# Kernel tuning notes

Hardware: AMD Instinct MI355X
Metric: run time of the kernel (lower is better)

The kernel has to match this reference:

```python
import jax, jax.numpy as jnp
import numpy as np

E = 128          # out_embedding_size
N = 128          # n_atoms
B = 512          # batch
CUTOFF = 5.0
LOG_STD_MIN, LOG_STD_MAX = -20.0, 2.0


def shifted_softplus(x):
    return jax.nn.softplus(x) - jnp.log(2.0).astype(x.dtype)


def cosine_cutoff(r):
    # SchNetPack CosineCutoff: 0.5*(cos(pi*r/rc)+1) for r < rc, else 0
    return 0.5 * (jnp.cos(r * (jnp.pi / CUTOFF)) + 1.0) * (r < CUTOFF).astype(r.dtype)


def setup_inputs() -> dict:
    key = jax.random.key(0)
    ks = jax.random.split(key, 8)
    kx = jax.random.normal(ks[0], (B, N, 2 * E + 1), dtype=jnp.float32)
    positions = jax.random.uniform(ks[1], (B, N, 3), dtype=jnp.float32) * 10.0
    # prefix-ones atoms mask (molecules padded at the end), 64..128 real atoms
    num_atoms = jax.random.randint(ks[2], (B,), 64, N + 1)
    atoms_mask = (jnp.arange(N)[None, :] < num_atoms[:, None]).astype(jnp.float32)
    eval_actions = jax.random.normal(ks[3], (B, N, 3), dtype=jnp.float32) * 0.1
    Wx = jax.random.normal(ks[4], (E, E), dtype=jnp.float32) / np.sqrt(E)
    bx = jnp.zeros((E,), dtype=jnp.float32)
    Wk = jax.random.normal(ks[5], (E, E), dtype=jnp.float32) / np.sqrt(E)
    bk = jnp.zeros((E,), dtype=jnp.float32)
    return {
        "kx": kx, "positions": positions, "atoms_mask": atoms_mask,
        "action_scale": jnp.float32(1.0), "eval_actions": eval_actions,
        "Wx": Wx, "bx": bx, "Wk": Wk, "bk": bk,
    }


def reference(kx, positions, atoms_mask, action_scale, eval_actions, Wx, bx, Wk, bk):
    kx = kx * atoms_mask[..., None]
    # P[b,i,j] = pos[b,j] - pos[b,i]
    P = positions[:, None, :, :] - positions[:, :, None, :]
    # safe norm: tiny eps inside sqrt so grads are finite on the zero diagonal
    r_ij = jnp.sqrt(jnp.sum(P * P, axis=-1) + 1e-16)
    P = P / (r_ij[..., None] + 1e-8)

    x = kx[..., :E]
    k = kx[..., E:2 * E]
    actions_log_std = kx[..., 2 * E:]  # [B,N,1]

    x = shifted_softplus(x) @ Wx.T + bx
    k = jax.nn.relu(k) @ Wk.T + bk

    inv_sqrt_e = 1.0 / jnp.sqrt(jnp.float32(E))
    x = jnp.einsum('bie,bje->bij', x, x) * inv_sqrt_e
    x = (r_ij - x) * 0.5
    k = jnp.einsum('bie,bje->bij', k, k) * inv_sqrt_e
    f = x * k

    # neighborhood mask: first num_atoms rows/cols are 1 (vectorized get_nbh_mask)
    counts = jnp.sum(atoms_mask, axis=-1)              # [B]
    idx = jnp.arange(N, dtype=counts.dtype)
    valid = (idx[None, :] < counts[:, None]).astype(f.dtype)   # [B,N]
    nbh_mask = valid[:, :, None] * valid[:, None, :]           # [B,N,N]

    fcut = cosine_cutoff(r_ij) * nbh_mask
    # summation_order='to' -> sum over dim 1
    actions_mean = jnp.sum(P * (f * fcut)[..., None], axis=1)  # [B,N,3]

    # limit_actions: tanh renormalization
    actions_norm = jnp.sqrt(jnp.sum(actions_mean * actions_mean, axis=-1) + 1e-16) + 1e-8
    actions_mean = actions_mean / actions_norm[..., None] * jnp.tanh(actions_norm)[..., None]

    # training path with eval_actions supplied
    actions_log_std = jnp.clip(actions_log_std, LOG_STD_MIN, LOG_STD_MAX)
    mu = actions_mean * action_scale
    sigma = jnp.exp(actions_log_std) * action_scale   # [B,N,1], broadcasts
    actions = eval_actions
    log_prob = (-0.5 * jnp.square((actions - mu) / sigma)
                - jnp.log(sigma)
                - 0.5 * jnp.log(2.0 * jnp.pi))
    log_prob = log_prob * atoms_mask[..., None]
    log_prob = jnp.sum(log_prob, axis=(1, 2))[:, None]  # [B,1]

    actions = actions * atoms_mask[..., None]
    return actions, log_prob
```

## Files before the change

kernel.cpp:

```cpp
#include <hip/hip_runtime.h>
#include <math.h>

#define EDIM 128
#define NATOM 128
#define NBATCH 512
#define THREADS 1024
#define ROWLEN 257

typedef __attribute__((ext_vector_type(8))) short bf16x8;
typedef __attribute__((ext_vector_type(4))) float f32x4;
typedef __attribute__((ext_vector_type(4))) unsigned short u16x4;

__device__ __forceinline__ unsigned short f2bf(float f) {
    unsigned u = __float_as_uint(f);
    u += 0x7FFFu + ((u >> 16) & 1u);
    return (unsigned short)(u >> 16);
}
__device__ __forceinline__ unsigned short cvt1(float x) {
    unsigned r;
    asm("v_cvt_pk_bf16_f32 %0, %1, %1" : "=v"(r) : "v"(x));
    return (unsigned short)r;
}
__device__ __forceinline__ float fast_ssp(float x) {
    return fmaxf(x, 0.f) + __logf(1.f + __expf(-fabsf(x))) - 0.69314718055994531f;
}
__device__ __forceinline__ int swzp(int row, int cbyte, int phase) {
    return row * 256 + ((cbyte ^ phase) ^ ((row & 7) << 4));
}

#define PH 0
#define QH 32768

__global__ void wcvt_kernel(const float* __restrict__ Wx,
                            const float* __restrict__ Wk,
                            unsigned short* __restrict__ ws) {
    int g = blockIdx.x * 256 + threadIdx.x;
    const float* src = (g < 16384) ? Wx : Wk;
    ws[g] = f2bf(src[g & 16383]);
}

__global__ void __launch_bounds__(THREADS, 8)
gen_actions_kernel(const float* __restrict__ kx,
                   const float* __restrict__ pos,
                   const float* __restrict__ mask,
                   const float* __restrict__ scale_ptr,
                   const float* __restrict__ evala,
                   const float* __restrict__ bx,
                   const float* __restrict__ bk,
                   const unsigned short* __restrict__ ws,
                   float* __restrict__ out)
{
    extern __shared__ char lds[];
    __shared__ float posXs[NATOM], posYs[NATOM], posZs[NATOM], lsBs[NATOM];
    __shared__ float amBs[NATOM * 3];
    __shared__ float redBs[2];
    __shared__ int   cntBs[2];

    const int b = blockIdx.x;
    const int t = threadIdx.x;
    const int lane = t & 63;
    const int w = t >> 6;
    const int wr = w >> 2;
    const int wc = w & 3;
    const int l15 = lane & 15;
    const int l4  = lane >> 4;

    if (t < NATOM) {
        float m = mask[b * NATOM + t];
        unsigned long long bal = __ballot(m > 0.5f);
        if ((t & 63) == 0) cntBs[t >> 6] = __popcll(bal);
        const float* p = pos + ((size_t)b * NATOM + t) * 3;
        posXs[t] = p[0]; posYs[t] = p[1]; posZs[t] = p[2];
        lsBs[t] = kx[(size_t)b * (NATOM * ROWLEN) + t * ROWLEN + 2 * EDIM];
    }
    if (t < NATOM * 3) amBs[t] = 0.f;

    {
        const float* kb = kx + (size_t)b * (NATOM * ROWLEN);
        #pragma unroll
        for (int j = 0; j < 16; ++j) {
            const int row = (j * 16 + w) & 127;
            const bool isX = (j < 8);
            const float* src = kb + row * ROWLEN + (isX ? 0 : 128);
            float x0 = src[lane];
            float x1 = src[lane + 64];
            float a0 = isX ? fast_ssp(x0) : fmaxf(x0, 0.f);
            float a1 = isX ? fast_ssp(x1) : fmaxf(x1, 0.f);
            char* base = lds + (isX ? PH : QH);
            const int phase = isX ? 0 : 64;
            *(unsigned short*)(base + swzp(row, lane * 2, phase)) = cvt1(a0);
            *(unsigned short*)(base + swzp(row, (lane + 64) * 2, phase)) = cvt1(a1);
        }
    }
    __syncthreads();
    const int count = cntBs[0] + cntBs[1];

    const int n0 = wc * 32;
    const bool nact = (n0 < count);
    u16x4 xpk[2][2], kpk[2][2];
    if (nact) {
        #pragma unroll
        for (int mat = 0; mat < 2; ++mat) {
            const char* act = lds + (mat ? QH : PH);
            const int phase = mat ? 64 : 0;
            const unsigned short* WH = ws + mat * 16384;
            const float* bias = mat ? bk : bx;
            f32x4 acc[2][2] = {};
            for (int ks = 0; ks < 4; ++ks) {
                const int e0 = ks * 32 + l4 * 8;
                bf16x8 wh[2], ah[2];
                #pragma unroll
                for (int mf = 0; mf < 2; ++mf) {
                    int orow = wr * 32 + mf * 16 + l15;
                    wh[mf] = *(const bf16x8*)(WH + orow * 128 + e0);
                }
                #pragma unroll
                for (int nf = 0; nf < 2; ++nf) {
                    int jrow = n0 + nf * 16 + l15;
                    ah[nf] = *(const bf16x8*)(act + swzp(jrow, e0 * 2, phase));
                }
                #pragma unroll
                for (int mf = 0; mf < 2; ++mf)
                    #pragma unroll
                    for (int nf = 0; nf < 2; ++nf)
                        acc[mf][nf] = __builtin_amdgcn_mfma_f32_16x16x32_bf16(wh[mf], ah[nf], acc[mf][nf], 0, 0, 0);
            }
            #pragma unroll
            for (int mf = 0; mf < 2; ++mf) {
                int ob = wr * 32 + mf * 16 + l4 * 4;
                f32x4 b4 = *(const f32x4*)(bias + ob);
                #pragma unroll
                for (int nf = 0; nf < 2; ++nf) {
                    u16x4 hs;
                    #pragma unroll
                    for (int r = 0; r < 4; ++r) hs[r] = cvt1(acc[mf][nf][r] + b4[r]);
                    if (mat) kpk[mf][nf] = hs; else xpk[mf][nf] = hs;
                }
            }
        }
    }
    __syncthreads();
    if (nact) {
        #pragma unroll
        for (int mf = 0; mf < 2; ++mf) {
            int ob2 = (wr * 32 + mf * 16 + l4 * 4) * 2;
            #pragma unroll
            for (int nf = 0; nf < 2; ++nf) {
                int jrow = n0 + nf * 16 + l15;
                *(u16x4*)(lds + PH + swzp(jrow, ob2, 0))  = xpk[mf][nf];
                *(u16x4*)(lds + QH + swzp(jrow, ob2, 64)) = kpk[mf][nf];
            }
        }
    }
    __syncthreads();

    const int m0g = wr * 32;
    const int n0g = wc * 32;
    f32x4 gx[2][2] = {}, gk[2][2] = {};
    const bool active = (m0g < count) && (n0g < count);
    if (active) {
        for (int ks = 0; ks < 4; ++ks) {
            const int e0b = (ks * 32 + l4 * 8) * 2;
            bf16x8 aH[2], bH[2];
            #pragma unroll
            for (int mf = 0; mf < 2; ++mf)
                aH[mf] = *(const bf16x8*)(lds + PH + swzp(m0g + mf * 16 + l15, e0b, 0));
            #pragma unroll
            for (int nf = 0; nf < 2; ++nf)
                bH[nf] = *(const bf16x8*)(lds + PH + swzp(n0g + nf * 16 + l15, e0b, 0));
            #pragma unroll
            for (int mf = 0; mf < 2; ++mf)
                #pragma unroll
                for (int nf = 0; nf < 2; ++nf)
                    gx[mf][nf] = __builtin_amdgcn_mfma_f32_16x16x32_bf16(aH[mf], bH[nf], gx[mf][nf], 0, 0, 0);
        }
        for (int ks = 0; ks < 4; ++ks) {
            const int e0b = (ks * 32 + l4 * 8) * 2;
            bf16x8 aH[2], bH[2];
            #pragma unroll
            for (int mf = 0; mf < 2; ++mf)
                aH[mf] = *(const bf16x8*)(lds + QH + swzp(m0g + mf * 16 + l15, e0b, 64));
            #pragma unroll
            for (int nf = 0; nf < 2; ++nf)
                bH[nf] = *(const bf16x8*)(lds + QH + swzp(n0g + nf * 16 + l15, e0b, 64));
            #pragma unroll
            for (int mf = 0; mf < 2; ++mf)
                #pragma unroll
                for (int nf = 0; nf < 2; ++nf)
                    gk[mf][nf] = __builtin_amdgcn_mfma_f32_16x16x32_bf16(aH[mf], bH[nf], gk[mf][nf], 0, 0, 0);
        }
        const float inv_e = 0.08838834764831845f;
        #pragma unroll
        for (int nf = 0; nf < 2; ++nf) {
            const int j = n0g + nf * 16 + l15;
            const bool jvalid = (j < count);
            const float pjx = posXs[j], pjy = posYs[j], pjz = posZs[j];
            float amx = 0.f, amy = 0.f, amz = 0.f;
            #pragma unroll
            for (int mf = 0; mf < 2; ++mf) {
                #pragma unroll
                for (int r = 0; r < 4; ++r) {
                    const int i = m0g + mf * 16 + l4 * 4 + r;
                    float dx = pjx - posXs[i];
                    float dy = pjy - posYs[i];
                    float dz = pjz - posZs[i];
                    float r2 = fmaf(dx, dx, fmaf(dy, dy, dz * dz)) + 1e-16f;
                    float rr = sqrtf(r2);
                    bool ok = jvalid && (i < count) && (rr < 5.0f);
                    float fc = ok ? (0.5f * (__cosf(rr * 0.62831853071795865f) + 1.f)) : 0.f;
                    float xs = fmaf(gx[mf][nf][r], -0.044194173824159216f, rr * 0.5f);
                    float fv = xs * (gk[mf][nf][r] * inv_e) * fc;
                    float wgt = fv / (rr + 1e-8f);
                    amx = fmaf(dx, wgt, amx);
                    amy = fmaf(dy, wgt, amy);
                    amz = fmaf(dz, wgt, amz);
                }
            }
            amx += __shfl_xor(amx, 16); amx += __shfl_xor(amx, 32);
            amy += __shfl_xor(amy, 16); amy += __shfl_xor(amy, 32);
            amz += __shfl_xor(amz, 16); amz += __shfl_xor(amz, 32);
            if (l4 == 0 && jvalid) {
                atomicAdd(&amBs[j * 3 + 0], amx);
                atomicAdd(&amBs[j * 3 + 1], amy);
                atomicAdd(&amBs[j * 3 + 2], amz);
            }
        }
    }
    __syncthreads();

    if (t < 96) {
        f32x4 ev4 = *(const f32x4*)(evala + (size_t)b * 384 + t * 4);
        f32x4 o4;
        #pragma unroll
        for (int c = 0; c < 4; ++c) {
            int atom = (t * 4 + c) / 3;
            o4[c] = (atom < count) ? ev4[c] : 0.f;
        }
        *(f32x4*)(out + (size_t)b * 384 + t * 4) = o4;
    }
    float lp = 0.f;
    if (t < NATOM && t < count) {
        const float* ev = evala + ((size_t)b * NATOM + t) * 3;
        float e0v = ev[0], e1v = ev[1], e2v = ev[2];
        float scale = scale_ptr[0];
        float ax = amBs[t * 3 + 0], ay = amBs[t * 3 + 1], az = amBs[t * 3 + 2];
        float nrm = sqrtf(fmaf(ax, ax, fmaf(ay, ay, az * az)) + 1e-16f) + 1e-8f;
        float qe = __expf(-2.f * nrm);
        float th = (1.f - qe) / (1.f + qe);
        float sc = th / nrm * scale;
        float ls = fminf(fmaxf(lsBs[t], -20.f), 2.f);
        float sig = __expf(ls) * scale;
        float sinv = 1.f / sig;
        float zx = (e0v - ax * sc) * sinv;
        float zy = (e1v - ay * sc) * sinv;
        float zz = (e2v - az * sc) * sinv;
        lp = -0.5f * (zx * zx + zy * zy + zz * zz) - 3.f * __logf(sig)
             - 3.f * 0.91893853320467274f;
    }
    #pragma unroll
    for (int off = 32; off > 0; off >>= 1) lp += __shfl_down(lp, off);
    if (t == 0)  redBs[0] = lp;
    if (t == 64) redBs[1] = lp;
    __syncthreads();
    if (t == 0) out[(size_t)NBATCH * NATOM * 3 + b] = redBs[0] + redBs[1];
}

extern "C" void kernel_launch(void* const* d_in, const int* in_sizes, int n_in,
                              void* d_out, int out_size, void* d_ws, size_t ws_size,
                              hipStream_t stream) {
    const float* kx    = (const float*)d_in[0];
    const float* pos   = (const float*)d_in[1];
    const float* mask  = (const float*)d_in[2];
    const float* scale = (const float*)d_in[3];
    const float* ev    = (const float*)d_in[4];
    const float* Wx    = (const float*)d_in[5];
    const float* bx    = (const float*)d_in[6];
    const float* Wk    = (const float*)d_in[7];
    const float* bk    = (const float*)d_in[8];
    float* out = (float*)d_out;
    unsigned short* ws = (unsigned short*)d_ws;

    hipLaunchKernelGGL(wcvt_kernel, dim3(128), dim3(256), 0, stream, Wx, Wk, ws);

    const size_t shbytes = 65536;
    (void)hipFuncSetAttribute((const void*)gen_actions_kernel,
                              hipFuncAttributeMaxDynamicSharedMemorySize,
                              (int)shbytes);
    hipLaunchKernelGGL(gen_actions_kernel, dim3(NBATCH), dim3(THREADS), shbytes, stream,
                       kx, pos, mask, scale, ev, bx, bk, ws, out);
}
```

Baseline: 54.76 us.

## Halve block to 512 threads with two M-tiles per wave

The block shrinks from 1024 to 512 threads (8 waves), and each wave now handles two 32-row output tiles in the projection GEMMs and the pairwise Gram GEMMs. The x and k projections are split into separate phases, each with its own barrier. The Gram stage reuses the B fragments across both M tiles and interleaves the x and k MFMAs. The intent is to cut per-block launch and barrier overhead and raise reuse per wave, at the cost of more registers per wave (launch bounds drop to 4) and one extra barrier.

```diff
diff --git a/kernel.cpp b/kernel.cpp
--- a/kernel.cpp
+++ b/kernel.cpp
@@ -4,7 +4,7 @@
 #define EDIM 128
 #define NATOM 128
 #define NBATCH 512
-#define THREADS 1024
+#define THREADS 512
 #define ROWLEN 257
 
 typedef __attribute__((ext_vector_type(8))) short bf16x8;
@@ -39,7 +39,7 @@
     ws[g] = f2bf(src[g & 16383]);
 }
 
-__global__ void __launch_bounds__(THREADS, 8)
+__global__ void __launch_bounds__(THREADS, 4)
 gen_actions_kernel(const float* __restrict__ kx,
                    const float* __restrict__ pos,
                    const float* __restrict__ mask,
@@ -60,7 +60,7 @@
     const int t = threadIdx.x;
     const int lane = t & 63;
     const int w = t >> 6;
-    const int wr = w >> 2;
+    const int wrb = w >> 2;
     const int wc = w & 3;
     const int l15 = lane & 15;
     const int l4  = lane >> 4;
@@ -77,10 +77,10 @@
 
     {
         const float* kb = kx + (size_t)b * (NATOM * ROWLEN);
-        #pragma unroll
-        for (int j = 0; j < 16; ++j) {
-            const int row = (j * 16 + w) & 127;
-            const bool isX = (j < 8);
+        #pragma unroll 4
+        for (int j = 0; j < 32; ++j) {
+            const int row = (j * 8 + w) & 127;
+            const bool isX = (j < 16);
             const float* src = kb + row * ROWLEN + (isX ? 0 : 128);
             float x0 = src[lane];
             float x1 = src[lane + 64];
@@ -97,97 +97,95 @@
 
     const int n0 = wc * 32;
     const bool nact = (n0 < count);
-    u16x4 xpk[2][2], kpk[2][2];
-    if (nact) {
-        #pragma unroll
-        for (int mat = 0; mat < 2; ++mat) {
-            const char* act = lds + (mat ? QH : PH);
-            const int phase = mat ? 64 : 0;
-            const unsigned short* WH = ws + mat * 16384;
-            const float* bias = mat ? bk : bx;
-            f32x4 acc[2][2] = {};
-            for (int ks = 0; ks < 4; ++ks) {
-                const int e0 = ks * 32 + l4 * 8;
-                bf16x8 wh[2], ah[2];
-                #pragma unroll
-                for (int mf = 0; mf < 2; ++mf) {
-                    int orow = wr * 32 + mf * 16 + l15;
-                    wh[mf] = *(const bf16x8*)(WH + orow * 128 + e0);
-                }
-                #pragma unroll
-                for (int nf = 0; nf < 2; ++nf) {
-                    int jrow = n0 + nf * 16 + l15;
-                    ah[nf] = *(const bf16x8*)(act + swzp(jrow, e0 * 2, phase));
-                }
-                #pragma unroll
-                for (int mf = 0; mf < 2; ++mf)
-                    #pragma unroll
-                    for (int nf = 0; nf < 2; ++nf)
-                        acc[mf][nf] = __builtin_amdgcn_mfma_f32_16x16x32_bf16(wh[mf], ah[nf], acc[mf][nf], 0, 0, 0);
-            }
-            #pragma unroll
-            for (int mf = 0; mf < 2; ++mf) {
-                int ob = wr * 32 + mf * 16 + l4 * 4;
-                f32x4 b4 = *(const f32x4*)(bias + ob);
-                #pragma unroll
-                for (int nf = 0; nf < 2; ++nf) {
-                    u16x4 hs;
-                    #pragma unroll
-                    for (int r = 0; r < 4; ++r) hs[r] = cvt1(acc[mf][nf][r] + b4[r]);
-                    if (mat) kpk[mf][nf] = hs; else xpk[mf][nf] = hs;
-                }
-            }
-        }
-    }
-    __syncthreads();
-    if (nact) {
-        #pragma unroll
-        for (int mf = 0; mf < 2; ++mf) {
-            int ob2 = (wr * 32 + mf * 16 + l4 * 4) * 2;
+
+    #define GEMM_MAT(MAT, PLANE, PHASE, WSOFF, BIAS)                                    \
+    {                                                                                   \
+        u16x4 pk[2][2][2];                                                              \
+        if (nact) {                                                                     \
+            const char* act = lds + PLANE;                                              \
+            const unsigned short* WH = ws + WSOFF;                                      \
+            f32x4 acc[2][2][2] = {};                                                    \
+            for (int ks = 0; ks < 4; ++ks) {                                            \
+                const int e0 = ks * 32 + l4 * 8;                                        \
+                bf16x8 ah[2];                                                           \
+                _Pragma("unroll")                                                       \
+                for (int nf = 0; nf < 2; ++nf)                                          \
+                    ah[nf] = *(const bf16x8*)(act + swzp(n0 + nf * 16 + l15, e0 * 2, PHASE)); \
+                _Pragma("unroll")                                                       \
+                for (int p = 0; p < 2; ++p) {                                           \
+                    _Pragma("unroll")                                                   \
+                    for (int mf = 0; mf < 2; ++mf) {                                    \
+                        int orow = (wrb + 2 * p) * 32 + mf * 16 + l15;                  \
+                        bf16x8 wh = *(const bf16x8*)(WH + orow * 128 + e0);             \
+                        _Pragma("unroll")                                               \
+                        for (int nf = 0; nf < 2; ++nf)                                  \
+                            acc[p][mf][nf] = __builtin_amdgcn_mfma_f32_16x16x32_bf16(wh, ah[nf], acc[p][mf][nf], 0, 0, 0); \
+                    }                                                                   \
+                }                                                                       \
+            }                                                                           \
+            _Pragma("unroll")                                                           \
+            for (int p = 0; p < 2; ++p)                                                 \
+                _Pragma("unroll")                                                       \
+                for (int mf = 0; mf < 2; ++mf) {                                        \
+                    int ob = (wrb + 2 * p) * 32 + mf * 16 + l4 * 4;                     \
+                    f32x4 b4 = *(const f32x4*)(BIAS + ob);                              \
+                    _Pragma("unroll")                                                   \
+                    for (int nf = 0; nf < 2; ++nf) {                                    \
+                        u16x4 hs;                                                       \
+                        _Pragma("unroll")                                               \
+                        for (int r = 0; r < 4; ++r) hs[r] = cvt1(acc[p][mf][nf][r] + b4[r]); \
+                        pk[p][mf][nf] = hs;                                             \
+                    }                                                                   \
+                }                                                                       \
+        }                                                                               \
+        __syncthreads();                      \
+        if (nact) {                                                                     \
+            _Pragma("unroll")                                                           \
+            for (int p = 0; p < 2; ++p)                                                 \
+                _Pragma("unroll")                                                       \
+                for (int mf = 0; mf < 2; ++mf) {                                        \
+                    int ob2 = ((wrb + 2 * p) * 32 + mf * 16 + l4 * 4) * 2;              \
+                    _Pragma("unroll")                                                   \
+                    for (int nf = 0; nf < 2; ++nf) {                                    \
+                        int jrow = n0 + nf * 16 + l15;                                  \
+                        *(u16x4*)(lds + PLANE + swzp(jrow, ob2, PHASE)) = pk[p][mf][nf]; \
+                    }                                                                   \
+                }                                                                       \
+        }                                                                               \
+    }
+
+    GEMM_MAT(0, PH, 0,  0,     bx)
+    GEMM_MAT(1, QH, 64, 16384, bk)
+    __syncthreads();
+
+    const int n0g = n0;
+    if (n0g < count) {
+        f32x4 gx[2][2][2] = {}, gk[2][2][2] = {};
+        for (int ks = 0; ks < 4; ++ks) {
+            const int e0b = (ks * 32 + l4 * 8) * 2;
+            bf16x8 bX[2], bK[2];
             #pragma unroll
             for (int nf = 0; nf < 2; ++nf) {
-                int jrow = n0 + nf * 16 + l15;
-                *(u16x4*)(lds + PH + swzp(jrow, ob2, 0))  = xpk[mf][nf];
-                *(u16x4*)(lds + QH + swzp(jrow, ob2, 64)) = kpk[mf][nf];
-            }
-        }
-    }
-    __syncthreads();
-
-    const int m0g = wr * 32;
-    const int n0g = wc * 32;
-    f32x4 gx[2][2] = {}, gk[2][2] = {};
-    const bool active = (m0g < count) && (n0g < count);
-    if (active) {
-        for (int ks = 0; ks < 4; ++ks) {
-            const int e0b = (ks * 32 + l4 * 8) * 2;
-            bf16x8 aH[2], bH[2];
+                bX[nf] = *(const bf16x8*)(lds + PH + swzp(n0g + nf * 16 + l15, e0b, 0));
+                bK[nf] = *(const bf16x8*)(lds + QH + swzp(n0g + nf * 16 + l15, e0b, 64));
+            }
             #pragma unroll
-            for (int mf = 0; mf < 2; ++mf)
-                aH[mf] = *(const bf16x8*)(lds + PH + swzp(m0g + mf * 16 + l15, e0b, 0));
-            #pragma unroll
-            for (int nf = 0; nf < 2; ++nf)
-                bH[nf] = *(const bf16x8*)(lds + PH + swzp(n0g + nf * 16 + l15, e0b, 0));
-            #pragma unroll
-            for (int mf = 0; mf < 2; ++mf)
-                #pragma unroll
-                for (int nf = 0; nf < 2; ++nf)
-                    gx[mf][nf] = __builtin_amdgcn_mfma_f32_16x16x32_bf16(aH[mf], bH[nf], gx[mf][nf], 0, 0, 0);
-        }
-        for (int ks = 0; ks < 4; ++ks) {
-            const int e0b = (ks * 32 + l4 * 8) * 2;
-            bf16x8 aH[2], bH[2];
-            #pragma unroll
-            for (int mf = 0; mf < 2; ++mf)
-                aH[mf] = *(const bf16x8*)(lds + QH + swzp(m0g + mf * 16 + l15, e0b, 64));
-            #pragma unroll
-            for (int nf = 0; nf < 2; ++nf)
-                bH[nf] = *(const bf16x8*)(lds + QH + swzp(n0g + nf * 16 + l15, e0b, 64));
-            #pragma unroll
-            for (int mf = 0; mf < 2; ++mf)
-                #pragma unroll
-                for (int nf = 0; nf < 2; ++nf)
-                    gk[mf][nf] = __builtin_amdgcn_mfma_f32_16x16x32_bf16(aH[mf], bH[nf], gk[mf][nf], 0, 0, 0);
+            for (int p = 0; p < 2; ++p) {
+                const int m0g = (wrb + 2 * p) * 32;
+                if (m0g < count) {
+                    #pragma unroll
+                    for (int mf = 0; mf < 2; ++mf) {
+                        int irow = m0g + mf * 16 + l15;
+                        bf16x8 aX = *(const bf16x8*)(lds + PH + swzp(irow, e0b, 0));
+                        bf16x8 aK = *(const bf16x8*)(lds + QH + swzp(irow, e0b, 64));
+                        #pragma unroll
+                        for (int nf = 0; nf < 2; ++nf) {
+                            gx[p][mf][nf] = __builtin_amdgcn_mfma_f32_16x16x32_bf16(aX, bX[nf], gx[p][mf][nf], 0, 0, 0);
+                            gk[p][mf][nf] = __builtin_amdgcn_mfma_f32_16x16x32_bf16(aK, bK[nf], gk[p][mf][nf], 0, 0, 0);
+                        }
+                    }
+                }
+            }
         }
         const float inv_e = 0.08838834764831845f;
         #pragma unroll
@@ -197,23 +195,29 @@
             const float pjx = posXs[j], pjy = posYs[j], pjz = posZs[j];
             float amx = 0.f, amy = 0.f, amz = 0.f;
             #pragma unroll
-            for (int mf = 0; mf < 2; ++mf) {
-                #pragma unroll
-                for (int r = 0; r < 4; ++r) {
-                    const int i = m0g + mf * 16 + l4 * 4 + r;
-                    float dx = pjx - posXs[i];
-                    float dy = pjy - posYs[i];
-                    float dz = pjz - posZs[i];
-                    float r2 = fmaf(dx, dx, fmaf(dy, dy, dz * dz)) + 1e-16f;
-                    float rr = sqrtf(r2);
-                    bool ok = jvalid && (i < count) && (rr < 5.0f);
-                    float fc = ok ? (0.5f * (__cosf(rr * 0.62831853071795865f) + 1.f)) : 0.f;
-                    float xs = fmaf(gx[mf][nf][r], -0.044194173824159216f, rr * 0.5f);
-                    float fv = xs * (gk[mf][nf][r] * inv_e) * fc;
-                    float wgt = fv / (rr + 1e-8f);
-                    amx = fmaf(dx, wgt, amx);
-                    amy = fmaf(dy, wgt, amy);
-                    amz = fmaf(dz, wgt, amz);
+            for (int p = 0; p < 2; ++p) {
+                const int m0g = (wrb + 2 * p) * 32;
+                if (m0g < count) {
+                    #pragma unroll
+                    for (int mf = 0; mf < 2; ++mf) {
+                        #pragma unroll
+                        for (int r = 0; r < 4; ++r) {
+                            const int i = m0g + mf * 16 + l4 * 4 + r;
+                            float dx = pjx - posXs[i];
+                            float dy = pjy - posYs[i];
+                            float dz = pjz - posZs[i];
+                            float r2 = fmaf(dx, dx, fmaf(dy, dy, dz * dz)) + 1e-16f;
+                            float rr = sqrtf(r2);
+                            bool ok = jvalid && (i < count) && (rr < 5.0f);
+                            float fc = ok ? (0.5f * (__cosf(rr * 0.62831853071795865f) + 1.f)) : 0.f;
+                            float xs = fmaf(gx[p][mf][nf][r], -0.044194173824159216f, rr * 0.5f);
+                            float fv = xs * (gk[p][mf][nf][r] * inv_e) * fc;
+                            float wgt = fv / (rr + 1e-8f);
+                            amx = fmaf(dx, wgt, amx);
+                            amy = fmaf(dy, wgt, amy);
+                            amz = fmaf(dz, wgt, amz);
+                        }
+                    }
                 }
             }
             amx += __shfl_xor(amx, 16); amx += __shfl_xor(amx, 32);
```

Result: faster. 53.09 us (-3.0%).
